# Optimization experiments

Hardware: AMD Instinct MI355X
Metric: run time of the kernel (lower is better)

The kernel has to match this reference:

```python
import jax, jax.numpy as jnp
import numpy as np

L = 16  # block size; g = c // L; lc = c // g


def linear(x, W, b):
    # x: [..., in], W: [in, out], b: [out]
    return jnp.dot(x, W) + b


def setup_inputs() -> dict:
    key = jax.random.key(0)
    ks = jax.random.split(key, 20)
    c = 256
    L2 = L * L
    s = 0.02
    inp = {"x": jax.random.normal(ks[0], (4, 32, 32, 32, c), dtype=jnp.float32)}
    names = [("W_h", (c, c)), ("b_h", (c,)), ("W_w", (c, c)), ("b_w", (c,)),
             ("W_c", (c, c)), ("b_c", (c,)), ("W_d", (c, c)), ("b_d", (c,)),
             ("W_attn", (L2, L2)), ("b_attn", (L2,)),
             ("W_1", (c, c)), ("b_1", (c,)), ("W_2", (c, c)), ("b_2", (c,)),
             ("W_3", (c, c)), ("b_3", (c,))]
    for i, (nm, shp) in enumerate(names):
        inp[nm] = jax.random.normal(ks[i + 1], shp, dtype=jnp.float32) * s
    return inp


def ip_mlp(x, W_h, b_h, W_w, b_w, W_c, b_c, W_attn, b_attn, W_1, b_1):
    b, h, w, d, c = x.shape
    g = c // L
    lc = c // g
    h1, w1 = h // L, w // L
    # x_att: b (h1 lh) (w1 lw) d c -> b h1 w1 d c (lh lw)
    xa = x.reshape(b, h1, L, w1, L, d, c).transpose(0, 1, 3, 5, 6, 2, 4)
    xa = xa.reshape(b, h1, w1, d, c, L * L)
    xa = linear(xa, W_attn, b_attn)
    xa = xa.reshape(b, h1, w1, d, c, L, L).transpose(0, 1, 5, 2, 6, 3, 4)
    x_att = xa.reshape(b, h, w, d, c)
    # x_h: b (h1 lh) w d (lc g) -> b (h1 w) lc d (lh g)
    xh = x.reshape(b, h1, L, w, d, lc, g).transpose(0, 1, 3, 5, 4, 2, 6)
    xh = xh.reshape(b, h1 * w, lc, d, L * g)
    xh = linear(xh, W_h, b_h)
    xh = xh.reshape(b, h1, w, lc, d, L, g).transpose(0, 1, 5, 2, 4, 3, 6)
    x_h = xh.reshape(b, h, w, d, c)
    # x_w: b h (w1 lw) d (lc g) -> b (h w1) lc d (lw g)
    xw = x.reshape(b, h, w1, L, d, lc, g).transpose(0, 1, 2, 5, 4, 3, 6)
    xw = xw.reshape(b, h * w1, lc, d, L * g)
    xw = linear(xw, W_w, b_w)
    xw = xw.reshape(b, h, w1, lc, d, L, g).transpose(0, 1, 2, 5, 4, 3, 6)
    x_w = xw.reshape(b, h, w, d, c)
    x_c = linear(x, W_c, b_c)
    out = (1.0 + x_att) * (x_h + x_w + x_c)
    return linear(out, W_1, b_1)


def tp_mlp(x, W_d, b_d, W_2, b_2):
    b, h, w, d, c = x.shape
    g = c // L
    l = c // g
    d1 = d // L
    # b h w (d1 ld) (l g) -> b h w d1 l (ld g)
    xd = x.reshape(b, h, w, d1, L, l, g).transpose(0, 1, 2, 3, 5, 4, 6)
    xd = xd.reshape(b, h, w, d1, l, L * g)
    xd = linear(xd, W_d, b_d)
    xd = xd.reshape(b, h, w, d1, l, L, g).transpose(0, 1, 2, 3, 5, 4, 6)
    xd = xd.reshape(b, h, w, d, c)
    return linear(xd, W_2, b_2)


def reference(x, W_h, b_h, W_w, b_w, W_c, b_c, W_d, b_d, W_attn, b_attn,
              W_1, b_1, W_2, b_2, W_3, b_3):
    x = x + ip_mlp(x, W_h, b_h, W_w, b_w, W_c, b_c, W_attn, b_attn, W_1, b_1)
    x = x + tp_mlp(x, W_d, b_d, W_2, b_2)
    x = x + linear(x, W_3, b_3)
    return x
```

## Files before the change

### kernel.cpp

```cpp
#include <hip/hip_runtime.h>


typedef __attribute__((ext_vector_type(8))) short bf16x8;
typedef __attribute__((ext_vector_type(8))) unsigned short u16x8;
typedef __attribute__((ext_vector_type(4))) float f32x4;
typedef __attribute__((ext_vector_type(4))) unsigned short u16x4;
typedef unsigned short u16;
typedef unsigned int u32;

#define DEV __device__ __forceinline__

DEV u16 f2b(float f) {
  union { float f; u32 u; } v; v.f = f;
  u32 r = v.u + 0x7FFFu + ((v.u >> 16) & 1u);
  return (u16)(r >> 16);
}
DEV float b2f(u16 b) {
  union { u32 u; float f; } v; v.u = ((u32)b) << 16; return v.f;
}

DEV int lds_off(int row, int colByte) {
  return (row << 9) + (colByte ^ ((row & 31) << 4));
}
DEV int lds_off256(int row, int colByte) {
  return (row << 8) + (colByte ^ ((row & 15) << 4));
}
DEV bf16x8 ld_lds(const u16* lds, int row, int colByte) {
  return *(const bf16x8*)((const char*)lds + lds_off(row, colByte));
}
DEV bf16x8 ld_glb(const u16* g, int row, int kByte) {
  return *(const bf16x8*)((const char*)g + (row << 9) + kByte);
}
DEV void stf4_nt(float* p, f32x4 v) { __builtin_nontemporal_store(v, (f32x4*)p); }

template <int MI, int NJ>
DEV void zero_acc(f32x4 acc[MI][NJ]) {
#pragma unroll
  for (int i = 0; i < MI; ++i)
#pragma unroll
    for (int j = 0; j < NJ; ++j) {
      acc[i][j][0] = 0.f; acc[i][j][1] = 0.f; acc[i][j][2] = 0.f; acc[i][j][3] = 0.f;
    }
}

template <int MI, int NJ, typename LA, typename LB>
DEV void gemmT(LA loadA, LB loadB, f32x4 acc[MI][NJ]) {
#pragma unroll
  for (int kk = 0; kk < 8; ++kk) {
    bf16x8 a[MI], b[NJ];
#pragma unroll
    for (int i = 0; i < MI; ++i) a[i] = loadA(i, kk);
#pragma unroll
    for (int j = 0; j < NJ; ++j) b[j] = loadB(j, kk);
#pragma unroll
    for (int i = 0; i < MI; ++i)
#pragma unroll
      for (int j = 0; j < NJ; ++j)
        acc[i][j] = __builtin_amdgcn_mfma_f32_16x16x32_bf16(a[i], b[j], acc[i][j], 0, 0, 0);
  }
}

#define WAVE_SETUP                  \
  const int tid = threadIdx.x;      \
  const int lane = tid & 63;        \
  const int wave = tid >> 6;        \
  const int wm = wave >> 2;         \
  const int wn = wave & 3;          \
  const int lr = lane & 15;         \
  const int lk = lane >> 4;

__global__ void k_pack_all(const float* W0, const float* W1p, const float* W2p,
                           const float* W3p, const float* W4p, const float* W5p,
                           const float* W6p, const float* W7p, u16* __restrict__ WT) {
  int bi = blockIdx.x;
  int wsel = bi >> 8, n = bi & 255;
  const float* W;
  switch (wsel) {
    case 0: W = W0; break; case 1: W = W1p; break; case 2: W = W2p; break;
    case 3: W = W3p; break; case 4: W = W4p; break; case 5: W = W5p; break;
    case 6: W = W6p; break; default: W = W7p; break;
  }
  u16* dst = WT + wsel * 65536;
  int k0 = threadIdx.x * 4;
#pragma unroll
  for (int i = 0; i < 4; ++i) {
    int k = k0 + i;
    float v = __builtin_nontemporal_load(W + k * 256 + n);
    if (wsel == 7 && k == n) v += 1.0f;
    dst[n * 256 + k] = f2b(v);
  }
}

__global__ __launch_bounds__(512, 4) void k_att(const float* __restrict__ x,
    const u16* __restrict__ WTattn, const float* __restrict__ b_attn,
    u16* __restrict__ att, u16* __restrict__ xbf) {
  __shared__ alignas(16) u16 XT[32768];
  WAVE_SETUP;
  const int ch = blockIdx.x & 1;
  const int t = blockIdx.x >> 1;
  const int d = t & 31, w1 = (t >> 5) & 1, h1 = (t >> 6) & 1, b = t >> 7;
  const int B0 = (((b * 32 + h1 * 16) * 32 + w1 * 16) * 32 + d) * 256;

  for (int i = tid; i < 4096; i += 512) {
    int cloc = i & 127;
    int q8 = i >> 7;
    u16x8 pk;
#pragma unroll
    for (int jj = 0; jj < 8; ++jj) {
      int q = q8 * 8 + jj;
      pk[jj] = f2b(x[B0 + (q >> 4) * 262144 + (q & 15) * 8192 + ch * 128 + cloc]);
    }
    *(u16x8*)((char*)XT + lds_off(cloc, q8 * 16)) = pk;
  }
  for (int i = tid; i < 8192; i += 512) {
    int q = i >> 5;
    int c4 = (i & 31) << 2;
    const int gofs = B0 + (q >> 4) * 262144 + (q & 15) * 8192 + ch * 128 + c4;
    const f32x4 v = *(const f32x4*)(x + gofs);
    u16x4 pk;
    pk[0] = f2b(v[0]); pk[1] = f2b(v[1]); pk[2] = f2b(v[2]); pk[3] = f2b(v[3]);
    *(u16x4*)(xbf + gofs) = pk;
  }
  __syncthreads();

  f32x4 acc[8][2];
  zero_acc<8, 2>(acc);
  gemmT<8, 2>(
      [&](int i, int kk) { return ld_glb(WTattn, wm * 128 + i * 16 + lr, kk * 64 + lk * 16); },
      [&](int j, int kk) { return ld_lds(XT, wn * 32 + j * 16 + lr, kk * 64 + lk * 16); },
      acc);

  __syncthreads();
#pragma unroll
  for (int i = 0; i < 8; ++i)
#pragma unroll
    for (int j = 0; j < 2; ++j)
#pragma unroll
      for (int r = 0; r < 4; ++r) {
        int p = wm * 128 + i * 16 + lk * 4 + r;
        int cl = wn * 32 + j * 16 + lr;
        XT[lds_off256(p, cl * 2) >> 1] = f2b(acc[i][j][r] + b_attn[p]);
      }
  __syncthreads();
  u16* out = att + t * 65536;
  for (int i = tid; i < 4096; i += 512) {
    int p = i >> 4, sB = (i & 15) << 4;
    bf16x8 v = *(const bf16x8*)((const char*)XT + p * 256 + sB);
    int c8l = (sB ^ ((p & 15) << 4)) >> 1;
    *(bf16x8*)(out + p * 256 + ch * 128 + c8l) = v;
  }
}

__global__ __launch_bounds__(512, 1) void k_hw(const u16* __restrict__ xbf,
    const u16* __restrict__ WTh, const u16* __restrict__ WTw,
    u16* __restrict__ h_out, u16* __restrict__ w_out) {
  __shared__ alignas(16) u16 XS[65536];
  __shared__ alignas(16) u16 BB[16384];
  WAVE_SETUP;
  const int t = blockIdx.x;
  const int d = t & 31, w1 = (t >> 5) & 1, h1 = (t >> 6) & 1, b = t >> 7;
  const int B0 = (((b * 32 + h1 * 16) * 32 + w1 * 16) * 32 + d) * 256;
  u16* h_t = h_out + t * 65536;
  u16* w_t = w_out + t * 65536;

  for (int i = tid; i < 8192; i += 512) {
    int pos = i >> 5, c8 = (i & 31) << 3;
    u16x8 v = *(const u16x8*)(xbf + B0 + (pos >> 4) * 262144 + (pos & 15) * 8192 + c8);
    *(u16x8*)((char*)XS + lds_off(pos, c8 * 2)) = v;
  }
  __syncthreads();

  for (int s = 0; s < 4; ++s) {
    f32x4 hacc[8][1];
    zero_acc<8, 1>(hacc);
    gemmT<8, 1>(
        [&](int i, int kk) {
          int k = kk * 32 + lk * 8;
          return *(const bf16x8*)((const char*)XS +
                                  lds_off((k >> 4) * 16 + lr, (wm * 8 + i) * 32 + (k & 15) * 2));
        },
        [&](int j, int kk) { return ld_glb(WTh, s * 64 + wn * 16 + lr, kk * 64 + lk * 16); },
        hacc);
    __syncthreads();
#pragma unroll
    for (int i = 0; i < 8; ++i)
#pragma unroll
      for (int r = 0; r < 4; ++r)
        BB[lds_off(wn * 16 + lk * 4 + r, ((wm * 8 + i) * 16 + lr) * 2) >> 1] = f2b(hacc[i][0][r]);
    __syncthreads();
    for (int i2 = tid; i2 < 2048; i2 += 512) {
      int posl = i2 >> 5, sB = (i2 & 31) << 4;
      bf16x8 v = *(const bf16x8*)((const char*)BB + posl * 512 + sB);
      int c8 = (sB ^ ((posl & 31) << 4)) >> 1;
      *(bf16x8*)(h_t + (s * 64 + posl) * 256 + c8) = v;
    }
  }

  for (int q = 0; q < 4; ++q) {
    f32x4 wacc[8][1];
    zero_acc<8, 1>(wacc);
    gemmT<8, 1>(
        [&](int i, int kk) {
          int k = kk * 32 + lk * 8;
          return *(const bf16x8*)((const char*)XS +
                                  lds_off(lr * 16 + (k >> 4), (wm * 8 + i) * 32 + (k & 15) * 2));
        },
        [&](int j, int kk) { return ld_glb(WTw, q * 64 + wn * 16 + lr, kk * 64 + lk * 16); },
        wacc);
    __syncthreads();
#pragma unroll
    for (int i = 0; i < 8; ++i)
#pragma unroll
      for (int r = 0; r < 4; ++r)
        BB[lds_off((lk * 4 + r) * 4 + wn, ((wm * 8 + i) * 16 + lr) * 2) >> 1] = f2b(wacc[i][0][r]);
    __syncthreads();
    for (int i2 = tid; i2 < 2048; i2 += 512) {
      int rb = i2 >> 5, sB = (i2 & 31) << 4;
      bf16x8 v = *(const bf16x8*)((const char*)BB + rb * 512 + sB);
      int c8 = (sB ^ ((rb & 31) << 4)) >> 1;
      int pos = (rb >> 2) * 16 + 4 * q + (rb & 3);
      *(bf16x8*)(w_t + pos * 256 + c8) = v;
    }
  }
}

__global__ __launch_bounds__(512, 2) void k_comb(const u16* __restrict__ xbf,
    const u16* __restrict__ h_out, const u16* __restrict__ w_out, const u16* __restrict__ att,
    const float* __restrict__ bh, const float* __restrict__ bw, const float* __restrict__ bc,
    const u16* __restrict__ WTc, const u16* __restrict__ WT1, const float* __restrict__ b1,
    u16* __restrict__ x1) {
  __shared__ alignas(16) u16 T[32768];
  WAVE_SETUP;
  const int ph = blockIdx.x & 1;
  const int t = blockIdx.x >> 1;
  const int d = t & 31, w1 = (t >> 5) & 1, h1 = (t >> 6) & 1, b = t >> 7;
  const int B0 = (((b * 32 + h1 * 16) * 32 + w1 * 16) * 32 + d) * 256;
  const u16* h_t = h_out + t * 65536;
  const u16* w_t = w_out + t * 65536;
  const u16* att_t = att + t * 65536;

  for (int i = tid; i < 4096; i += 512) {
    int posl = i >> 5, c8 = (i & 31) << 3;
    int pos = ph * 128 + posl;
    u16x8 v = *(const u16x8*)(xbf + B0 + (pos >> 4) * 262144 + (pos & 15) * 8192 + c8);
    *(u16x8*)((char*)T + lds_off(posl, c8 * 2)) = v;
  }
  __syncthreads();

  f32x4 acc[4][4];
  zero_acc<4, 4>(acc);
  gemmT<4, 4>(
      [&](int i, int kk) { return ld_lds(T, wm * 64 + i * 16 + lr, kk * 64 + lk * 16); },
      [&](int j, int kk) { return ld_glb(WTc, wn * 64 + j * 16 + lr, kk * 64 + lk * 16); },
      acc);
  __syncthreads();

#pragma unroll
  for (int i = 0; i < 4; ++i) {
    int lh = ph * 8 + wm * 4 + i;
#pragma unroll
    for (int j = 0; j < 4; ++j) {
      float bcv = bc[wn * 64 + j * 16 + lr];
#pragma unroll
      for (int r = 0; r < 4; ++r) {
        int posl = wm * 64 + i * 16 + lk * 4 + r;
        int n = wn * 64 + j * 16 + lr;
        float v = acc[i][j][r] + bcv + bh[lh * 16 + lr] + bw[(lk * 4 + r) * 16 + lr];
        T[lds_off(posl, n * 2) >> 1] = f2b(v);
      }
    }
  }
  __syncthreads();

  for (int i2 = tid; i2 < 4096; i2 += 512) {
    int posl = i2 >> 5, c8 = (i2 & 31) << 3;
    int pos = ph * 128 + posl;
    u16x8 hv = *(const u16x8*)(h_t + pos * 256 + c8);
    u16x8 wv = *(const u16x8*)(w_t + pos * 256 + c8);
    u16x8 av = *(const u16x8*)(att_t + pos * 256 + c8);
    u16x8* p = (u16x8*)((char*)T + lds_off(posl, c8 * 2));
    u16x8 cur = *p, o;
#pragma unroll
    for (int j = 0; j < 8; ++j)
      o[j] = f2b((1.0f + b2f(av[j])) * (b2f(cur[j]) + b2f(hv[j]) + b2f(wv[j])));
    *p = o;
  }
  __syncthreads();

  zero_acc<4, 4>(acc);
  gemmT<4, 4>(
      [&](int i, int kk) { return ld_lds(T, wm * 64 + i * 16 + lr, kk * 64 + lk * 16); },
      [&](int j, int kk) { return ld_glb(WT1, wn * 64 + j * 16 + lr, kk * 64 + lk * 16); },
      acc);
  __syncthreads();

#pragma unroll
  for (int i = 0; i < 4; ++i)
#pragma unroll
    for (int j = 0; j < 4; ++j) {
      float b1v = b1[wn * 64 + j * 16 + lr];
#pragma unroll
      for (int r = 0; r < 4; ++r) {
        int posl = wm * 64 + i * 16 + lk * 4 + r;
        int n = wn * 64 + j * 16 + lr;
        T[lds_off(posl, n * 2) >> 1] = f2b(acc[i][j][r] + b1v);
      }
    }
  __syncthreads();

  for (int i2 = tid; i2 < 4096; i2 += 512) {
    int posl = i2 >> 5, sB = (i2 & 31) << 4;
    bf16x8 v = *(const bf16x8*)((const char*)T + posl * 512 + sB);
    int c8 = (sB ^ ((posl & 31) << 4)) >> 1;
    int pos = ph * 128 + posl;
    const int gofs = B0 + (pos >> 4) * 262144 + (pos & 15) * 8192 + c8;
    u16x8 xv = *(const u16x8*)(xbf + gofs);
    u16x8 o;
#pragma unroll
    for (int j = 0; j < 8; ++j) o[j] = f2b(b2f((u16)v[j]) + b2f(xv[j]));
    *(u16x8*)(x1 + gofs) = o;
  }
}

__global__ __launch_bounds__(512, 2) void k_tp(const u16* __restrict__ x1,
    const u16* __restrict__ WTd, const u16* __restrict__ WT2, const u16* __restrict__ WT3p,
    const float* __restrict__ bd, const float* __restrict__ b2, const float* __restrict__ b3,
    float* __restrict__ outp) {
  __shared__ alignas(16) u16 T[32768];
  WAVE_SETUP;
  const int bid = blockIdx.x;
  const int wg = bid & 3, d1 = (bid >> 2) & 1, h = (bid >> 3) & 31, b = bid >> 8;
  const int W0 = (b * 32 + h) * 32 + wg * 8;

  u16x8 xkeep[8];
#pragma unroll
  for (int u = 0; u < 8; ++u) {
    int i = tid + u * 512;
    int Rl = i >> 5, c8 = (i & 31) << 3;
    const u16x8 v = *(const u16x8*)(x1 + (size_t)(W0 + (Rl >> 4)) * 8192 +
                                    (d1 * 16 + (Rl & 15)) * 256 + c8);
    xkeep[u] = v;
    *(u16x8*)((char*)T + lds_off(Rl, c8 * 2)) = v;
  }
  __syncthreads();

  f32x4 acc[4][4];
  zero_acc<4, 4>(acc);
  gemmT<4, 4>(
      [&](int i, int kk) {
        int k = kk * 32 + lk * 8;
        int mt = wm * 4 + i;
        return *(const bf16x8*)((const char*)T + lds_off(mt * 16 + (k >> 4),
                                                         lr * 32 + (k & 15) * 2));
      },
      [&](int j, int kk) { return ld_glb(WTd, wn * 64 + j * 16 + lr, kk * 64 + lk * 16); },
      acc);
  __syncthreads();

#pragma unroll
  for (int i = 0; i < 4; ++i)
#pragma unroll
    for (int j = 0; j < 4; ++j)
#pragma unroll
      for (int r = 0; r < 4; ++r) {
        int mloc = wm * 64 + i * 16 + lk * 4 + r;
        int n = wn * 64 + j * 16 + lr;
        int row = ((mloc >> 4) << 4) + (n >> 4);
        int col = ((mloc & 15) << 4) + (n & 15);
        T[lds_off(row, col * 2) >> 1] = f2b(acc[i][j][r] + bd[n]);
      }
  __syncthreads();

  zero_acc<4, 4>(acc);
  gemmT<4, 4>(
      [&](int i, int kk) { return ld_lds(T, (wm * 4 + i) * 16 + lr, kk * 64 + lk * 16); },
      [&](int j, int kk) { return ld_glb(WT2, wn * 64 + j * 16 + lr, kk * 64 + lk * 16); },
      acc);
  __syncthreads();

#pragma unroll
  for (int i = 0; i < 4; ++i)
#pragma unroll
    for (int j = 0; j < 4; ++j) {
      float b2v = b2[wn * 64 + j * 16 + lr];
#pragma unroll
      for (int r = 0; r < 4; ++r) {
        int mloc = wm * 64 + i * 16 + lk * 4 + r;
        int n = wn * 64 + j * 16 + lr;
        T[lds_off(mloc, n * 2) >> 1] = f2b(acc[i][j][r] + b2v);
      }
    }
  __syncthreads();

#pragma unroll
  for (int u = 0; u < 8; ++u) {
    int i = tid + u * 512;
    int Rl = i >> 5, c8 = (i & 31) << 3;
    u16x8* p = (u16x8*)((char*)T + lds_off(Rl, c8 * 2));
    u16x8 cur = *p, o;
#pragma unroll
    for (int j = 0; j < 8; ++j) o[j] = f2b(b2f(cur[j]) + b2f(xkeep[u][j]));
    *p = o;
  }
  __syncthreads();

  zero_acc<4, 4>(acc);
  gemmT<4, 4>(
      [&](int i, int kk) { return ld_lds(T, (wm * 4 + i) * 16 + lr, kk * 64 + lk * 16); },
      [&](int j, int kk) { return ld_glb(WT3p, wn * 64 + j * 16 + lr, kk * 64 + lk * 16); },
      acc);

  float* Tf = (float*)T;
#pragma unroll
  for (int half = 0; half < 2; ++half) {
    __syncthreads();
    if (wm == half) {
#pragma unroll
      for (int i = 0; i < 4; ++i)
#pragma unroll
        for (int j = 0; j < 4; ++j)
#pragma unroll
          for (int r = 0; r < 4; ++r) {
            int row = i * 16 + lk * 4 + r;
            int n = wn * 64 + j * 16 + lr;
            Tf[row * 256 + n] = acc[i][j][r] + b3[n];
          }
    }
    __syncthreads();
    for (int i2 = tid; i2 < 4096; i2 += 512) {
      int row = i2 >> 6, c4 = (i2 & 63) << 2;
      int Rg = half * 64 + row;
      f32x4 v = *(const f32x4*)(Tf + row * 256 + c4);
      stf4_nt(outp + (size_t)(W0 + (Rg >> 4)) * 8192 + (d1 * 16 + (Rg & 15)) * 256 + c4, v);
    }
  }
}

extern "C" void kernel_launch(void* const* d_in, const int* in_sizes, int n_in,
                              void* d_out, int out_size, void* d_ws, size_t ws_size,
                              hipStream_t stream) {
  (void)in_sizes; (void)n_in; (void)out_size; (void)ws_size;
  const float* x      = (const float*)d_in[0];
  const float* W_h    = (const float*)d_in[1];
  const float* b_h    = (const float*)d_in[2];
  const float* W_w    = (const float*)d_in[3];
  const float* b_w    = (const float*)d_in[4];
  const float* W_c    = (const float*)d_in[5];
  const float* b_c    = (const float*)d_in[6];
  const float* W_d    = (const float*)d_in[7];
  const float* b_d    = (const float*)d_in[8];
  const float* W_attn = (const float*)d_in[9];
  const float* b_attn = (const float*)d_in[10];
  const float* W_1    = (const float*)d_in[11];
  const float* b_1    = (const float*)d_in[12];
  const float* W_2    = (const float*)d_in[13];
  const float* b_2    = (const float*)d_in[14];
  const float* W_3    = (const float*)d_in[15];
  const float* b_3    = (const float*)d_in[16];
  float* outp = (float*)d_out;

  u16* WT = (u16*)d_ws;
  u16* R1 = WT + 8 * 65536;
  u16* R2 = R1 + 33554432;
  u16* HOS = (u16*)d_out;
  u16* WOS = HOS + 33554432;

  k_pack_all<<<2048, 64, 0, stream>>>(W_h, W_w, W_c, W_attn, W_1, W_d, W_2, W_3, WT);

  k_att <<<1024, 512, 0, stream>>>(x, WT + 3 * 65536, b_attn, R2, R1);
  k_hw  <<<512, 512, 0, stream>>>(R1, WT + 0 * 65536, WT + 1 * 65536, HOS, WOS);
  k_comb<<<1024, 512, 0, stream>>>(R1, HOS, WOS, R2, b_h, b_w, b_c,
                                   WT + 2 * 65536, WT + 4 * 65536, b_1, R1);
  k_tp  <<<1024, 512, 0, stream>>>(R1, WT + 5 * 65536, WT + 6 * 65536, WT + 7 * 65536,
                                   b_d, b_2, b_3, outp);
}
```

Baseline: 520.9 us.

## Split k_hw blocks by channel half to halve LDS and double occupancy

The h/w grouped-projection kernel now splits each tile across two blocks by channel half (128 channels each), which halves the shared-memory staging buffers and the per-warp accumulator count. Launch bounds rise to two blocks per CU and the grid doubles to 1024 blocks. A new XOR swizzle is added for the 256-byte-row LDS layout to avoid bank conflicts on the transposed h/w access patterns. The aim is more latency hiding through occupancy; the cost is that each block re-reads the full weight matrices from global memory for only half the output work.

```diff
diff --git a/kernel.cpp b/kernel.cpp
--- a/kernel.cpp
+++ b/kernel.cpp
@@ -24,6 +24,9 @@
 }
 DEV int lds_off256(int row, int colByte) {
   return (row << 8) + (colByte ^ ((row & 15) << 4));
+}
+DEV int lds_offH(int row, int colByte) {
+  return (row << 8) + (colByte ^ (((row ^ (row >> 4)) & 15) << 4));
 }
 DEV bf16x8 ld_lds(const u16* lds, int row, int colByte) {
   return *(const bf16x8*)((const char*)lds + lds_off(row, colByte));
@@ -151,75 +154,79 @@
   }
 }
 
-__global__ __launch_bounds__(512, 1) void k_hw(const u16* __restrict__ xbf,
+__global__ __launch_bounds__(512, 2) void k_hw(const u16* __restrict__ xbf,
     const u16* __restrict__ WTh, const u16* __restrict__ WTw,
     u16* __restrict__ h_out, u16* __restrict__ w_out) {
-  __shared__ alignas(16) u16 XS[65536];
-  __shared__ alignas(16) u16 BB[16384];
+  __shared__ alignas(16) u16 XS[32768];
+  __shared__ alignas(16) u16 BB[8192];
   WAVE_SETUP;
-  const int t = blockIdx.x;
+  const int ch = blockIdx.x & 1;
+  const int t = blockIdx.x >> 1;
   const int d = t & 31, w1 = (t >> 5) & 1, h1 = (t >> 6) & 1, b = t >> 7;
   const int B0 = (((b * 32 + h1 * 16) * 32 + w1 * 16) * 32 + d) * 256;
-  u16* h_t = h_out + t * 65536;
-  u16* w_t = w_out + t * 65536;
-
-  for (int i = tid; i < 8192; i += 512) {
-    int pos = i >> 5, c8 = (i & 31) << 3;
-    u16x8 v = *(const u16x8*)(xbf + B0 + (pos >> 4) * 262144 + (pos & 15) * 8192 + c8);
-    *(u16x8*)((char*)XS + lds_off(pos, c8 * 2)) = v;
+  u16* h_t = h_out + t * 65536 + ch * 128;
+  u16* w_t = w_out + t * 65536 + ch * 128;
+
+  for (int i = tid; i < 4096; i += 512) {
+    int pos = i >> 4, c8 = (i & 15) << 3;
+    u16x8 v = *(const u16x8*)(xbf + B0 + (pos >> 4) * 262144 + (pos & 15) * 8192 +
+                              ch * 128 + c8);
+    *(u16x8*)((char*)XS + lds_offH(pos, c8 * 2)) = v;
   }
   __syncthreads();
 
   for (int s = 0; s < 4; ++s) {
-    f32x4 hacc[8][1];
-    zero_acc<8, 1>(hacc);
-    gemmT<8, 1>(
+    f32x4 hacc[4][1];
+    zero_acc<4, 1>(hacc);
+    gemmT<4, 1>(
         [&](int i, int kk) {
           int k = kk * 32 + lk * 8;
           return *(const bf16x8*)((const char*)XS +
-                                  lds_off((k >> 4) * 16 + lr, (wm * 8 + i) * 32 + (k & 15) * 2));
+                                  lds_offH((k >> 4) * 16 + lr, (wm * 4 + i) * 32 + (k & 15) * 2));
         },
         [&](int j, int kk) { return ld_glb(WTh, s * 64 + wn * 16 + lr, kk * 64 + lk * 16); },
         hacc);
     __syncthreads();
 #pragma unroll
-    for (int i = 0; i < 8; ++i)
+    for (int i = 0; i < 4; ++i)
 #pragma unroll
       for (int r = 0; r < 4; ++r)
-        BB[lds_off(wn * 16 + lk * 4 + r, ((wm * 8 + i) * 16 + lr) * 2) >> 1] = f2b(hacc[i][0][r]);
-    __syncthreads();
-    for (int i2 = tid; i2 < 2048; i2 += 512) {
-      int posl = i2 >> 5, sB = (i2 & 31) << 4;
-      bf16x8 v = *(const bf16x8*)((const char*)BB + posl * 512 + sB);
-      int c8 = (sB ^ ((posl & 31) << 4)) >> 1;
-      *(bf16x8*)(h_t + (s * 64 + posl) * 256 + c8) = v;
+        BB[lds_off256(wn * 16 + lk * 4 + r, ((wm * 4 + i) * 16 + lr) * 2) >> 1] =
+            f2b(hacc[i][0][r]);
+    __syncthreads();
+    for (int i2 = tid; i2 < 1024; i2 += 512) {
+      int posl = i2 >> 4, sB = (i2 & 15) << 4;
+      bf16x8 v = *(const bf16x8*)((const char*)BB + posl * 256 + sB);
+      int c8l = (sB ^ ((posl & 15) << 4)) >> 1;
+      *(bf16x8*)(h_t + (s * 64 + posl) * 256 + c8l) = v;
     }
   }
 
   for (int q = 0; q < 4; ++q) {
-    f32x4 wacc[8][1];
-    zero_acc<8, 1>(wacc);
-    gemmT<8, 1>(
+    f32x4 wacc[4][1];
+    zero_acc<4, 1>(wacc);
+    gemmT<4, 1>(
         [&](int i, int kk) {
           int k = kk * 32 + lk * 8;
           return *(const bf16x8*)((const char*)XS +
-                                  lds_off(lr * 16 + (k >> 4), (wm * 8 + i) * 32 + (k & 15) * 2));
+                                  lds_offH(lr * 16 + (k >> 4), (wm * 4 + i) * 32 + (k & 15) * 2));
         },
         [&](int j, int kk) { return ld_glb(WTw, q * 64 + wn * 16 + lr, kk * 64 + lk * 16); },
         wacc);
     __syncthreads();
 #pragma unroll
-    for (int i = 0; i < 8; ++i)
+    for (int i = 0; i < 4; ++i)
 #pragma unroll
       for (int r = 0; r < 4; ++r)
-        BB[lds_off((lk * 4 + r) * 4 + wn, ((wm * 8 + i) * 16 + lr) * 2) >> 1] = f2b(wacc[i][0][r]);
-    __syncthreads();
-    for (int i2 = tid; i2 < 2048; i2 += 512) {
-      int rb = i2 >> 5, sB = (i2 & 31) << 4;
-      bf16x8 v = *(const bf16x8*)((const char*)BB + rb * 512 + sB);
-      int c8 = (sB ^ ((rb & 31) << 4)) >> 1;
+        BB[lds_off256((lk * 4 + r) * 4 + wn, ((wm * 4 + i) * 16 + lr) * 2) >> 1] =
+            f2b(wacc[i][0][r]);
+    __syncthreads();
+    for (int i2 = tid; i2 < 1024; i2 += 512) {
+      int rb = i2 >> 4, sB = (i2 & 15) << 4;
+      bf16x8 v = *(const bf16x8*)((const char*)BB + rb * 256 + sB);
+      int c8l = (sB ^ ((rb & 15) << 4)) >> 1;
       int pos = (rb >> 2) * 16 + 4 * q + (rb & 3);
-      *(bf16x8*)(w_t + pos * 256 + c8) = v;
+      *(bf16x8*)(w_t + pos * 256 + c8l) = v;
     }
   }
 }
@@ -468,7 +475,7 @@
   k_pack_all<<<2048, 64, 0, stream>>>(W_h, W_w, W_c, W_attn, W_1, W_d, W_2, W_3, WT);
 
   k_att <<<1024, 512, 0, stream>>>(x, WT + 3 * 65536, b_attn, R2, R1);
-  k_hw  <<<512, 512, 0, stream>>>(R1, WT + 0 * 65536, WT + 1 * 65536, HOS, WOS);
+  k_hw  <<<1024, 512, 0, stream>>>(R1, WT + 0 * 65536, WT + 1 * 65536, HOS, WOS);
   k_comb<<<1024, 512, 0, stream>>>(R1, HOS, WOS, R2, b_h, b_w, b_c,
                                    WT + 2 * 65536, WT + 4 * 65536, b_1, R1);
   k_tp  <<<1024, 512, 0, stream>>>(R1, WT + 5 * 65536, WT + 6 * 65536, WT + 7 * 65536,
```

After: 490.1 us, median of 2. 1.06x faster.
